# Kernel optimization log

Measured on AMD Instinct MI355X. Metric: run time of the kernel, lower is better.

Reference implementation:

```python
import jax, jax.numpy as jnp
import numpy as np


def setup_inputs() -> dict:
    key = jax.random.key(0)
    ks = jax.random.split(key, 8)
    B, C, H, W = 4, 256, 56, 56
    Cq = C // 8
    s = 0.05  # small init scale for conv weights, like kaiming-ish for 1x1 convs
    return {
        "x": jax.random.normal(ks[0], (B, C, H, W), jnp.float32),
        "Wq": jax.random.normal(ks[1], (Cq, C), jnp.float32) * s,
        "bq": jax.random.normal(ks[2], (Cq,), jnp.float32) * s,
        "Wk": jax.random.normal(ks[3], (Cq, C), jnp.float32) * s,
        "bk": jax.random.normal(ks[4], (Cq,), jnp.float32) * s,
        "Wv": jax.random.normal(ks[5], (C, C), jnp.float32) * s,
        "bv": jax.random.normal(ks[6], (C,), jnp.float32) * s,
        "gamma": jax.random.normal(ks[7], (1,), jnp.float32),
    }


def reference(x, Wq, bq, Wk, bk, Wv, bv, gamma):
    B, C, H, W = x.shape
    N = H * W
    xf = x.reshape(B, C, N)  # flatten spatial

    # 1x1 convs == channel matmuls
    q = jnp.einsum('oc,bcn->bon', Wq, xf) + bq[None, :, None]   # [B,Cq,N]
    k = jnp.einsum('oc,bcn->bon', Wk, xf) + bk[None, :, None]   # [B,Cq,N]
    v = jnp.einsum('oc,bcn->bon', Wv, xf) + bv[None, :, None]   # [B,C,N]

    # lipschitz_norm from weights: u=||Q||_F, v=max row-norm of K^T, w=max row-norm of V^T
    u = jnp.linalg.norm(Wq)
    vn = jnp.max(jnp.linalg.norm(Wk.T, axis=1))
    wn = jnp.max(jnp.linalg.norm(Wv.T, axis=1))
    norm_value = jnp.maximum(u * vn, u * wn)  # maximum(u*v, v*u, u*w)

    # energy[b,i,j] = <q[:,i], k[:,j]>, scaled by custom Lipschitz norm
    energy = jnp.einsum('bci,bcj->bij', q, k) / norm_value      # [B,N,N]
    attention = jax.nn.softmax(energy, axis=-1)

    # out[b,c,i] = sum_j v[b,c,j] * attention[b,i,j]
    out = jnp.einsum('bcj,bij->bci', v, attention).reshape(B, C, H, W)

    # lipschitz_bound: exp(sqrt(3)) * sqrt(N/C) + 2*sqrt(6)
    bound = np.float32(np.exp(np.sqrt(3.0)) * np.sqrt(N / C) + 2.0 * np.sqrt(6.0))
    out = out / bound

    return gamma * out + x
```

## Files before the change

### kernel.cpp

```cpp
#include <hip/hip_runtime.h>

#define N_SP 3136
#define C_CH 256
#define CQ   32
#define NB   4
#define JT   64
#define NJT  49
#define QT   128
#define NQT  25
#define JSPL 2
#define INV_BOUND 0.04051569f
#define LOG2E 1.44269504f

typedef __attribute__((ext_vector_type(8))) short bf16x8;
typedef __attribute__((ext_vector_type(4))) float f32x4;
typedef __attribute__((ext_vector_type(2))) long long l64x2;
typedef unsigned short u16;
typedef unsigned int   u32;
typedef unsigned char  u8;
typedef long long      l64;

#define MFMA16(a,b,c) __builtin_amdgcn_mfma_f32_16x16x32_bf16(a,b,c,0,0,0)
#define MFMA8(a,b,c)  __builtin_amdgcn_mfma_f32_16x16x32_bf8_fp8(a,b,c,0,0,0)

__device__ __forceinline__ u16 f2b(float f) {
    u32 u = __builtin_bit_cast(u32, f);
    u += 0x7fffu + ((u >> 16) & 1u);
    return (u16)(u >> 16);
}
__device__ __forceinline__ float b2f(u16 v) {
    return __builtin_bit_cast(float, (u32)v << 16);
}
__device__ __forceinline__ u8 f2fp8(float f) {
    return (u8)(__builtin_amdgcn_cvt_pk_fp8_f32(f, f, 0, false) & 0xff);
}
__device__ __forceinline__ void dma16(const void* g, void* l) {
    __builtin_amdgcn_global_load_lds((const __attribute__((address_space(1))) u32*)g,
                                     (__attribute__((address_space(3))) u32*)l, 16, 0, 0);
}
__device__ __forceinline__ void dma4(const void* g, void* l) {
    __builtin_amdgcn_global_load_lds((const __attribute__((address_space(1))) u32*)g,
                                     (__attribute__((address_space(3))) u32*)l, 4, 0, 0);
}

__global__ __launch_bounds__(256) void stage1_kernel(
    const float* __restrict__ x, const float* __restrict__ Wq,
    const float* __restrict__ Wk, const float* __restrict__ Wv,
    u8* __restrict__ xT, u8* __restrict__ Wqb, u8* __restrict__ Wkb,
    u8* __restrict__ Wvb, float* __restrict__ scale_out,
    float* __restrict__ kmax)
{
    __shared__ float smem[64 * 65];
    const int t = threadIdx.x;
    const int bid = blockIdx.x;

    if (bid < 784) {
        float (*tile)[65] = (float(*)[65])smem;
        const int ct = bid & 3, nt = (bid >> 2) % 49, b = bid / 196;
        const int c0 = ct * 64, n0 = nt * 64;
        const int cc = t >> 4, nn4 = (t & 15) * 4;
        #pragma unroll
        for (int k = 0; k < 4; ++k) {
            int cl = cc + k * 16;
            float4 v = *(const float4*)(x + (size_t)(b * C_CH + c0 + cl) * N_SP + n0 + nn4);
            tile[cl][nn4] = v.x; tile[cl][nn4 + 1] = v.y;
            tile[cl][nn4 + 2] = v.z; tile[cl][nn4 + 3] = v.w;
        }
        __syncthreads();
        const int c4 = (t & 15) * 4, nn = t >> 4;
        #pragma unroll
        for (int k = 0; k < 4; ++k) {
            int nl = nn + k * 16;
            ushort4 o;
            o.x = f2b(tile[c4 + 0][nl]); o.y = f2b(tile[c4 + 1][nl]);
            o.z = f2b(tile[c4 + 2][nl]); o.w = f2b(tile[c4 + 3][nl]);
            const int off = ((c0 + c4) * 2) ^ ((nl & 15) << 5);
            *(ushort4*)(xT + (size_t)(b * N_SP + n0 + nl) * 512 + off) = o;
        }
    } else if (bid < 864) {
        int idx = (bid - 784) * 256 + t;
        const float* src; u8* dst; int off;
        if (idx < 2048)      { src = Wq; dst = Wqb; off = idx; }
        else if (idx < 4096) { src = Wk; dst = Wkb; off = idx - 2048; }
        else                 { src = Wv; dst = Wvb; off = idx - 4096; }
        float4 v = *(const float4*)(src + off * 4);
        ushort4 o; o.x = f2b(v.x); o.y = f2b(v.y); o.z = f2b(v.z); o.w = f2b(v.w);
        const int row = off >> 6, inner = (off & 63) * 8;
        *(ushort4*)(dst + row * 512 + (inner ^ ((row & 15) << 5))) = o;
    } else {
        if (t < NB) kmax[t] = 0.f;
        float* red = smem;
        float u2 = 0.f;
        for (int i = t; i < CQ * C_CH; i += 256) { float w = Wq[i]; u2 += w * w; }
        red[t] = u2; __syncthreads();
        #pragma unroll
        for (int s = 128; s > 0; s >>= 1) { if (t < s) red[t] += red[t + s]; __syncthreads(); }
        float u2t = red[0]; __syncthreads();
        float vn2 = 0.f;
        for (int o = 0; o < CQ; ++o)   { float w = Wk[o * C_CH + t]; vn2 += w * w; }
        float wn2 = 0.f;
        for (int o = 0; o < C_CH; ++o) { float w = Wv[o * C_CH + t]; wn2 += w * w; }
        red[t] = fmaxf(vn2, wn2); __syncthreads();
        #pragma unroll
        for (int s = 128; s > 0; s >>= 1) { if (t < s) red[t] = fmaxf(red[t], red[t + s]); __syncthreads(); }
        if (t == 0) scale_out[0] = 1.0f / (sqrtf(u2t) * sqrtf(red[0]));
    }
}

__global__ __launch_bounds__(256) void qkv_mfma(
    const u8* __restrict__ xT, const u8* __restrict__ Wqb,
    const u8* __restrict__ Wkb, const u8* __restrict__ Wvb,
    const float* __restrict__ bq, const float* __restrict__ bk,
    const float* __restrict__ bv, const float* __restrict__ scale_p,
    u16* __restrict__ qT, u8* __restrict__ Kg, u8* __restrict__ Vg,
    float* __restrict__ qnorm, float* __restrict__ kmax)
{
    __shared__ __align__(16) u8 xTl[32768];
    __shared__ __align__(16) u8 Wl[32768];

    const int t = threadIdx.x;
    const int split = blockIdx.x / 196, tile = blockIdx.x % 196;
    const int b = tile / 49, nt = tile % 49;
    const int w = t >> 6, lane = t & 63, li = t & 15, g = (t >> 4) & 3;
    const int n = nt * 64 + w * 16 + li;
    const int r0 = (split - 1) * 64;
    const f32x4 zero = {0.f, 0.f, 0.f, 0.f};

    {
        const u8* xsrc = xT + (size_t)(b * N_SP + nt * 64) * 512;
        #pragma unroll
        for (int i = 0; i < 8; ++i)
            dma16(xsrc + w * 8192 + i * 1024 + lane * 16, xTl + w * 8192 + i * 1024);
        if (split == 0) {
            #pragma unroll
            for (int i = 0; i < 4; ++i)
                dma16(Wqb + w * 4096 + i * 1024 + lane * 16, Wl + w * 4096 + i * 1024);
            #pragma unroll
            for (int i = 0; i < 4; ++i)
                dma16(Wkb + w * 4096 + i * 1024 + lane * 16, Wl + 16384 + w * 4096 + i * 1024);
        } else {
            const u8* wsrc = Wvb + (size_t)r0 * 512;
            #pragma unroll
            for (int i = 0; i < 8; ++i)
                dma16(wsrc + w * 8192 + i * 1024 + lane * 16, Wl + w * 8192 + i * 1024);
        }
    }
    asm volatile("s_waitcnt vmcnt(0)" ::: "memory");
    __syncthreads();

    const int swz = li << 5;
    bf16x8 xf[8];
    #pragma unroll
    for (int ks = 0; ks < 8; ++ks)
        xf[ks] = *(const bf16x8*)(xTl + (w * 16 + li) * 512 + ((ks * 64 + 16 * g) ^ swz));

    if (split == 0) {
        f32x4 aq0 = zero, aq1 = zero, ak0 = zero, ak1 = zero;
        #pragma unroll
        for (int ks = 0; ks < 8; ++ks) {
            const int o = (ks * 64 + 16 * g) ^ swz;
            bf16x8 w0 = *(const bf16x8*)(Wl + li * 512 + o);
            bf16x8 w1 = *(const bf16x8*)(Wl + (16 + li) * 512 + o);
            bf16x8 w2 = *(const bf16x8*)(Wl + 16384 + li * 512 + o);
            bf16x8 w3 = *(const bf16x8*)(Wl + 16384 + (16 + li) * 512 + o);
            aq0 = MFMA16(w0, xf[ks], aq0);
            aq1 = MFMA16(w1, xf[ks], aq1);
            ak0 = MFMA16(w2, xf[ks], ak0);
            ak1 = MFMA16(w3, xf[ks], ak1);
        }
        const float scf = scale_p[0] * LOG2E;
        f32x4 bq0 = *(const f32x4*)(bq + 4 * g);
        f32x4 bq1 = *(const f32x4*)(bq + 16 + 4 * g);
        f32x4 bk0 = *(const f32x4*)(bk + 4 * g);
        f32x4 bk1 = *(const f32x4*)(bk + 16 + 4 * g);
        float qn2 = 0.f, kn2 = 0.f;
        ushort4 s0, s1;
        #pragma unroll
        for (int r = 0; r < 4; ++r) {
            float q0 = (aq0[r] + bq0[r]) * scf;
            float q1 = (aq1[r] + bq1[r]) * scf;
            qn2 += q0 * q0 + q1 * q1;
            ((u16*)&s0)[r] = f2b(q0); ((u16*)&s1)[r] = f2b(q1);
        }
        *(ushort4*)(qT + (size_t)(b * N_SP + n) * CQ + 4 * g)      = s0;
        *(ushort4*)(qT + (size_t)(b * N_SP + n) * CQ + 16 + 4 * g) = s1;
        #pragma unroll
        for (int r = 0; r < 4; ++r) {
            float k0 = ak0[r] + bk0[r];
            float k1 = ak1[r] + bk1[r];
            kn2 += k0 * k0 + k1 * k1;
            ((u16*)&s0)[r] = f2b(k0); ((u16*)&s1)[r] = f2b(k1);
        }
        u8* krow = Kg + ((size_t)b * N_SP + n) * 64;
        const int swn = ((n >> 1) & 3) << 4;
        *(ushort4*)(krow + ((8 * g) ^ swn))      = s0;
        *(ushort4*)(krow + ((32 + 8 * g) ^ swn)) = s1;

        qn2 += __shfl_xor(qn2, 16); qn2 += __shfl_xor(qn2, 32);
        kn2 += __shfl_xor(kn2, 16); kn2 += __shfl_xor(kn2, 32);
        if (g == 0) qnorm[b * N_SP + n] = sqrtf(qn2);
        float kn = sqrtf(kn2);
        #pragma unroll
        for (int d = 1; d < 16; d <<= 1) kn = fmaxf(kn, __shfl_xor(kn, d));
        if ((t & 63) == 0) atomicMax((int*)(kmax + b), __float_as_int(kn));
    } else {
        f32x4 a[4] = {zero, zero, zero, zero};
        #pragma unroll
        for (int ks = 0; ks < 8; ++ks) {
            const int o = (ks * 64 + 16 * g) ^ swz;
            #pragma unroll
            for (int fr = 0; fr < 4; ++fr) {
                bf16x8 wf = *(const bf16x8*)(Wl + (fr * 16 + li) * 512 + o);
                a[fr] = MFMA16(wf, xf[ks], a[fr]);
            }
        }
        const int jj = w * 16 + li;
        const int p = ((jj >> 5) & 1) * 8 + ((jj >> 3) & 3) * 16 + (jj & 7);
        u8* vtile = Vg + (size_t)(b * NJT + nt) * 16384;
        #pragma unroll
        for (int fr = 0; fr < 4; ++fr) {
            f32x4 bb = *(const f32x4*)(bv + r0 + fr * 16 + 4 * g);
            #pragma unroll
            for (int r = 0; r < 4; ++r) {
                const int c = r0 + fr * 16 + 4 * g + r;
                vtile[c * 64 + (p ^ (((c >> 1) & 3) << 4))] = f2fp8(a[fr][r] + bb[r]);
            }
        }
    }
}

__global__ __launch_bounds__(512) void attn_mfma(
    const u16* __restrict__ qT, const u8* __restrict__ Kg,
    const u8* __restrict__ Vg, const float* __restrict__ qnorm,
    const float* __restrict__ kmax, u16* __restrict__ numP,
    float* __restrict__ lsP)
{
    __shared__ __align__(16) u8 smem[88064];
    u8* const Vl = smem;
    u8* const Kl = smem + 65536;
    u8* const Pl = smem + 81920;

    const int t = threadIdx.x;
    const int w = t >> 6, li = t & 15, g = (t >> 4) & 3;
    const int jh = w & 3, qh = w >> 2;
    const int cw = w * 32;
    const int swz = ((li >> 1) & 3) << 4;

    const int bid = blockIdx.x;
    const int b = bid / 50, rem = bid % 50;
    const int qt = rem >> 1, js = rem & 1;
    const int i0 = qt * QT;
    const int jbeg = js ? 25 : 0, jend = js ? 49 : 25;
    const int nIter = jend - jbeg;

    const u16* qTb = qT + (size_t)b * N_SP * CQ;
    const u8*  Kbb = Kg + (size_t)b * N_SP * 64;
    const u8*  Vbb = Vg + (size_t)b * NJT * 16384;
    const float kmb = kmax[b];
    const f32x4 zero = {0.f, 0.f, 0.f, 0.f};

    bf16x8 qf[4]; float mr[4];
    #pragma unroll
    for (int f = 0; f < 4; ++f) {
        int qr = i0 + (qh * 4 + f) * 16 + li;
        qr = qr < N_SP ? qr : N_SP - 1;
        qf[f] = *(const bf16x8*)(qTb + (size_t)qr * CQ + 8 * g);
        mr[f] = qnorm[b * N_SP + qr] * kmb;
    }

    f32x4 acc[8][2];
    #pragma unroll
    for (int qq = 0; qq < 8; ++qq) { acc[qq][0] = zero; acc[qq][1] = zero; }
    float ls4[4] = {0.f, 0.f, 0.f, 0.f};

    #define ISSUE(jt_, s_) do {                                               \
        const u8* vsrc_ = Vbb + (size_t)(jt_) * 16384;                        \
        const u8* ksrc_ = Kbb + (size_t)(jt_) * 4096;                         \
        _Pragma("unroll")                                                     \
        for (int i_ = 0; i_ < 2; ++i_)                                        \
            dma16(vsrc_ + i_ * 8192 + t * 16,                                 \
                  Vl + (s_) * 16384 + i_ * 8192 + w * 1024);                  \
        _Pragma("unroll")                                                     \
        for (int i_ = 0; i_ < 2; ++i_)                                        \
            dma4(ksrc_ + i_ * 2048 + t * 4,                                   \
                 Kl + (s_) * 4096 + i_ * 2048 + w * 256);                     \
    } while (0)

    ISSUE(jbeg, 0);
    ISSUE(jbeg + 1, 1);
    ISSUE(jbeg + 2, 2);

    const int p0 = ((jh >> 1) & 1) * 8 + ((jh * 2 + (g >> 1)) & 3) * 16 + 4 * (g & 1);

    for (int ii = 0; ii < nIter; ++ii) {
        const int it = jbeg + ii;
        const int cur = ii & 3;
        asm volatile("s_waitcnt vmcnt(8) lgkmcnt(0)" ::: "memory");
        __builtin_amdgcn_s_barrier();
        asm volatile("" ::: "memory");

        {
            int jn = it + 3; if (jn > jend - 1) jn = jend - 1;
            ISSUE(jn, (cur + 3) & 3);
        }

        const u8* Kc = Kl + cur * 4096;
        bf16x8 kf = *(const bf16x8*)(Kc + (jh * 16 + li) * 64 + ((16 * g) ^ swz));
        #pragma unroll
        for (int f = 0; f < 4; ++f) {
            f32x4 s = MFMA16(kf, qf[f], zero);
            float a0 = exp2f(s[0] - mr[f]), a1 = exp2f(s[1] - mr[f]);
            float a2 = exp2f(s[2] - mr[f]), a3 = exp2f(s[3] - mr[f]);
            ls4[f] += (a0 + a1) + (a2 + a3);
            int pk = __builtin_amdgcn_cvt_pk_bf8_f32(a0, a1, 0, false);
            pk = __builtin_amdgcn_cvt_pk_bf8_f32(a2, a3, pk, true);
            *(u32*)(Pl + ((qh * 4 + f) * 16 + li) * 64 + (p0 ^ swz)) = (u32)pk;
        }
        asm volatile("s_waitcnt lgkmcnt(0)" ::: "memory");
        __builtin_amdgcn_s_barrier();
        asm volatile("" ::: "memory");

        const u8* Vc = Vl + cur * 16384;
        __builtin_amdgcn_s_setprio(1);
        l64x2 v0 = *(const l64x2*)(Vc + (cw + li) * 64 + ((16 * g) ^ swz));
        l64x2 v1 = *(const l64x2*)(Vc + (cw + 16 + li) * 64 + ((16 * g) ^ swz));
        #pragma unroll
        for (int qq = 0; qq < 8; ++qq) {
            l64x2 pa = *(const l64x2*)(Pl + (qq * 16 + li) * 64 + ((16 * g) ^ swz));
            acc[qq][0] = MFMA8(pa[0], v0[0], acc[qq][0]);
            acc[qq][1] = MFMA8(pa[0], v1[0], acc[qq][1]);
            acc[qq][0] = MFMA8(pa[1], v0[1], acc[qq][0]);
            acc[qq][1] = MFMA8(pa[1], v1[1], acc[qq][1]);
        }
        __builtin_amdgcn_s_setprio(0);
    }
    #undef ISSUE

    #pragma unroll
    for (int f = 0; f < 4; ++f) {
        ls4[f] += __shfl_xor(ls4[f], 16);
        ls4[f] += __shfl_xor(ls4[f], 32);
    }
    __syncthreads();
    float* red = (float*)Pl;
    if ((t & 63) < 16) {
        #pragma unroll
        for (int f = 0; f < 4; ++f) red[w * 64 + f * 16 + li] = ls4[f];
    }
    __syncthreads();
    if (t < QT) {
        const int qh2 = t >> 6, rowin = t & 63;
        float s = red[(qh2 * 4 + 0) * 64 + rowin] + red[(qh2 * 4 + 1) * 64 + rowin]
                + red[(qh2 * 4 + 2) * 64 + rowin] + red[(qh2 * 4 + 3) * 64 + rowin];
        lsP[(size_t)bid * QT + t] = s;
    }

    u16* np = numP + (size_t)bid * QT * C_CH;
    #pragma unroll
    for (int qq = 0; qq < 8; ++qq) {
        #pragma unroll
        for (int cf = 0; cf < 2; ++cf) {
            const int c = cw + cf * 16 + li;
            ushort4 o;
            o.x = f2b(acc[qq][cf][0]); o.y = f2b(acc[qq][cf][1]);
            o.z = f2b(acc[qq][cf][2]); o.w = f2b(acc[qq][cf][3]);
            *(ushort4*)(np + c * QT + qq * 16 + 4 * g) = o;
        }
    }
}

__global__ __launch_bounds__(256) void attn_combine(
    const u16* __restrict__ numP, const float* __restrict__ lsP,
    const float* __restrict__ x, const float* __restrict__ gamma_p,
    float* __restrict__ out)
{
    const int bid = blockIdx.x;
    const int b = bid / 100, rem = bid % 100;
    const int qt = rem >> 2, qq4 = rem & 3;
    const int i0 = qt * QT;
    if (i0 + qq4 * 32 >= N_SP) return;

    const int t = threadIdx.x;
    const int q32 = t & 31, cg = t >> 5;
    const int qloc = qq4 * 32 + q32;
    const int qglob = i0 + qloc;

    const size_t blk0 = ((size_t)b * NQT + qt) * 2;
    const float lsf = lsP[blk0 * QT + qloc] + lsP[(blk0 + 1) * QT + qloc];
    const float rinv = gamma_p[0] * INV_BOUND / lsf;

    const u16* np0 = numP + blk0 * QT * C_CH;
    const u16* np1 = np0 + QT * C_CH;

    #pragma unroll 8
    for (int cc = 0; cc < 32; ++cc) {
        const int c = cg * 32 + cc;
        float num = b2f(np0[c * QT + qloc]) + b2f(np1[c * QT + qloc]);
        const size_t base = ((size_t)b * C_CH + c) * N_SP + qglob;
        out[base] = num * rinv + x[base];
    }
}

extern "C" void kernel_launch(void* const* d_in, const int* in_sizes, int n_in,
                              void* d_out, int out_size, void* d_ws, size_t ws_size,
                              hipStream_t stream)
{
    const float* x  = (const float*)d_in[0];
    const float* Wq = (const float*)d_in[1];
    const float* bq = (const float*)d_in[2];
    const float* Wk = (const float*)d_in[3];
    const float* bk = (const float*)d_in[4];
    const float* Wv = (const float*)d_in[5];
    const float* bv = (const float*)d_in[6];
    const float* gm = (const float*)d_in[7];
    float* out = (float*)d_out;
    float* ws  = (float*)d_ws;

    float* scale = ws;
    float* kmax  = ws + 4;
    float* qnorm = ws + 8;
    u8* Wqb = (u8*)(ws + 8 + NB * N_SP);
    u8* Wkb = Wqb + 32 * 512;
    u8* Wvb = Wkb + 32 * 512;
    u8* xT  = Wvb + 256 * 512;
    u16* qT = (u16*)(xT + (size_t)NB * N_SP * 512);
    u8* Kg  = (u8*)(qT + (size_t)NB * N_SP * CQ);
    u8* Vg  = Kg + (size_t)NB * N_SP * 64;
    u16* numP = (u16*)(Vg + (size_t)NB * NJT * 16384);
    float* lsP = (float*)(numP + (size_t)200 * QT * C_CH);

    stage1_kernel<<<865, 256, 0, stream>>>(x, Wq, Wk, Wv, xT, Wqb, Wkb, Wvb, scale, kmax);
    qkv_mfma<<<980, 256, 0, stream>>>(xT, Wqb, Wkb, Wvb, bq, bk, bv, scale, qT, Kg, Vg, qnorm, kmax);
    attn_mfma<<<200, 512, 0, stream>>>(qT, Kg, Vg, qnorm, kmax, numP, lsP);
    attn_combine<<<400, 256, 0, stream>>>(numP, lsP, x, gm, out);
}
```

Baseline: 93.84 us.

## Split attention key range four ways and shrink pipeline to three stages

Doubles the split-K factor of the attention kernel from 2 to 4, launching 400 blocks instead of 200 so more of the 256 CUs get work. LDS use drops from four to three K/V pipeline stages so more blocks can fit per CU, and the combine kernel now sums four partial numerators and denominators. The cost is twice the partial-output traffic in bf16, more combine work, and a shallower prefetch pipeline.

```diff
diff --git a/kernel.cpp b/kernel.cpp
--- a/kernel.cpp
+++ b/kernel.cpp
@@ -8,7 +8,7 @@
 #define NJT  49
 #define QT   128
 #define NQT  25
-#define JSPL 2
+#define JSPL 4
 #define INV_BOUND 0.04051569f
 #define LOG2E 1.44269504f
 
@@ -229,16 +229,16 @@
     }
 }
 
-__global__ __launch_bounds__(512) void attn_mfma(
+__global__ __launch_bounds__(512, 4) void attn_mfma(
     const u16* __restrict__ qT, const u8* __restrict__ Kg,
     const u8* __restrict__ Vg, const float* __restrict__ qnorm,
     const float* __restrict__ kmax, u16* __restrict__ numP,
     float* __restrict__ lsP)
 {
-    __shared__ __align__(16) u8 smem[88064];
+    __shared__ __align__(16) u8 smem[69632];
     u8* const Vl = smem;
-    u8* const Kl = smem + 65536;
-    u8* const Pl = smem + 81920;
+    u8* const Kl = smem + 49152;
+    u8* const Pl = smem + 61440;
 
     const int t = threadIdx.x;
     const int w = t >> 6, li = t & 15, g = (t >> 4) & 3;
@@ -247,10 +247,10 @@
     const int swz = ((li >> 1) & 3) << 4;
 
     const int bid = blockIdx.x;
-    const int b = bid / 50, rem = bid % 50;
-    const int qt = rem >> 1, js = rem & 1;
+    const int b = bid / 100, rem = bid % 100;
+    const int qt = rem >> 2, js = rem & 3;
     const int i0 = qt * QT;
-    const int jbeg = js ? 25 : 0, jend = js ? 49 : 25;
+    const int jbeg = (NJT * js) / 4, jend = (NJT * (js + 1)) / 4;
     const int nIter = jend - jbeg;
 
     const u16* qTb = qT + (size_t)b * N_SP * CQ;
@@ -288,20 +288,20 @@
 
     ISSUE(jbeg, 0);
     ISSUE(jbeg + 1, 1);
-    ISSUE(jbeg + 2, 2);
 
     const int p0 = ((jh >> 1) & 1) * 8 + ((jh * 2 + (g >> 1)) & 3) * 16 + 4 * (g & 1);
 
+    int cur = 0;
     for (int ii = 0; ii < nIter; ++ii) {
         const int it = jbeg + ii;
-        const int cur = ii & 3;
-        asm volatile("s_waitcnt vmcnt(8) lgkmcnt(0)" ::: "memory");
+        asm volatile("s_waitcnt vmcnt(4) lgkmcnt(0)" ::: "memory");
         __builtin_amdgcn_s_barrier();
         asm volatile("" ::: "memory");
 
         {
-            int jn = it + 3; if (jn > jend - 1) jn = jend - 1;
-            ISSUE(jn, (cur + 3) & 3);
+            int jn = it + 2; if (jn > jend - 1) jn = jend - 1;
+            int s2 = cur + 2; if (s2 >= 3) s2 -= 3;
+            ISSUE(jn, s2);
         }
 
         const u8* Kc = Kl + cur * 4096;
@@ -333,6 +333,8 @@
             acc[qq][1] = MFMA8(pa[1], v1[1], acc[qq][1]);
         }
         __builtin_amdgcn_s_setprio(0);
+
+        ++cur; if (cur == 3) cur = 0;
     }
     #undef ISSUE
 
@@ -375,27 +377,30 @@
     float* __restrict__ out)
 {
     const int bid = blockIdx.x;
-    const int b = bid / 100, rem = bid % 100;
-    const int qt = rem >> 2, qq4 = rem & 3;
+    const int b = bid / 50, rem = bid % 50;
+    const int qt = rem >> 1, hf = rem & 1;
     const int i0 = qt * QT;
-    if (i0 + qq4 * 32 >= N_SP) return;
 
     const int t = threadIdx.x;
-    const int q32 = t & 31, cg = t >> 5;
-    const int qloc = qq4 * 32 + q32;
+    const int qloc = hf * 64 + (t & 63), cg = t >> 6;
     const int qglob = i0 + qloc;
-
-    const size_t blk0 = ((size_t)b * NQT + qt) * 2;
-    const float lsf = lsP[blk0 * QT + qloc] + lsP[(blk0 + 1) * QT + qloc];
+    if (qglob >= N_SP) return;
+
+    const size_t blk0 = ((size_t)b * NQT + qt) * 4;
+    float lsf = 0.f;
+    #pragma unroll
+    for (int s = 0; s < 4; ++s) lsf += lsP[(blk0 + s) * QT + qloc];
     const float rinv = gamma_p[0] * INV_BOUND / lsf;
 
-    const u16* np0 = numP + blk0 * QT * C_CH;
-    const u16* np1 = np0 + QT * C_CH;
+    const u16* np = numP + blk0 * (size_t)(QT * C_CH);
 
     #pragma unroll 8
-    for (int cc = 0; cc < 32; ++cc) {
-        const int c = cg * 32 + cc;
-        float num = b2f(np0[c * QT + qloc]) + b2f(np1[c * QT + qloc]);
+    for (int cc = 0; cc < 64; ++cc) {
+        const int c = cg * 64 + cc;
+        float num = b2f(np[c * QT + qloc])
+                  + b2f(np[1 * QT * C_CH + c * QT + qloc])
+                  + b2f(np[2 * QT * C_CH + c * QT + qloc])
+                  + b2f(np[3 * QT * C_CH + c * QT + qloc]);
         const size_t base = ((size_t)b * C_CH + c) * N_SP + qglob;
         out[base] = num * rinv + x[base];
     }
@@ -427,10 +432,10 @@
     u8* Kg  = (u8*)(qT + (size_t)NB * N_SP * CQ);
     u8* Vg  = Kg + (size_t)NB * N_SP * 64;
     u16* numP = (u16*)(Vg + (size_t)NB * NJT * 16384);
-    float* lsP = (float*)(numP + (size_t)200 * QT * C_CH);
+    float* lsP = (float*)(numP + (size_t)400 * QT * C_CH);
 
     stage1_kernel<<<865, 256, 0, stream>>>(x, Wq, Wk, Wv, xT, Wqb, Wkb, Wvb, scale, kmax);
     qkv_mfma<<<980, 256, 0, stream>>>(xT, Wqb, Wkb, Wvb, bq, bk, bv, scale, qT, Kg, Vg, qnorm, kmax);
-    attn_mfma<<<200, 512, 0, stream>>>(qT, Kg, Vg, qnorm, kmax, numP, lsP);
-    attn_combine<<<400, 256, 0, stream>>>(numP, lsP, x, gm, out);
-}
+    attn_mfma<<<NB * NQT * JSPL, 512, 0, stream>>>(qT, Kg, Vg, qnorm, kmax, numP, lsP);
+    attn_combine<<<NB * NQT * 2, 256, 0, stream>>>(numP, lsP, x, gm, out);
+}
```

New measurement: 95.58 us. About the same (+1.9%).
